# Optimization experiments

Hardware: AMD Instinct MI355X
Metric: run time of the kernel (lower is better)

## Reference

```python
import jax, jax.numpy as jnp
import numpy as np

B, TF, TP = 32, 2048, 256
FRAME_DIM, PHN_DIM, ATT_DIM = 768, 512, 512
LN_EPS = 1e-5


def setup_inputs() -> dict:
    key = jax.random.key(0)
    ks = jax.random.split(key, 9)
    frame_hidden = jax.random.normal(ks[0], (B, TF, FRAME_DIM), dtype=jnp.float32)
    phn_hidden = jax.random.normal(ks[1], (B, TP, PHN_DIM), dtype=jnp.float32)
    labels_att_mask = jax.random.randint(ks[2], (B, TP), 0, 2, dtype=jnp.int32)
    # ensure every row has at least one attended phoneme position
    labels_att_mask = labels_att_mask.at[:, 0].set(1)
    s_q = 1.0 / np.sqrt(FRAME_DIM)
    s_k = 1.0 / np.sqrt(PHN_DIM)
    Wq = jax.random.uniform(ks[3], (FRAME_DIM, ATT_DIM), jnp.float32, -s_q, s_q)
    bq = jax.random.uniform(ks[4], (ATT_DIM,), jnp.float32, -s_q, s_q)
    Wk = jax.random.uniform(ks[5], (PHN_DIM, ATT_DIM), jnp.float32, -s_k, s_k)
    bk = jax.random.uniform(ks[6], (ATT_DIM,), jnp.float32, -s_k, s_k)
    gamma = jnp.ones((2 * ATT_DIM,), jnp.float32)
    beta = jnp.zeros((2 * ATT_DIM,), jnp.float32)
    return {"frame_hidden": frame_hidden, "phn_hidden": phn_hidden,
            "labels_att_mask": labels_att_mask,
            "Wq": Wq, "bq": bq, "Wk": Wk, "bk": bk,
            "gamma": gamma, "beta": beta}


def _layer_norm(x, gamma, beta):
    mu = jnp.mean(x, axis=-1, keepdims=True)
    var = jnp.mean(jnp.square(x - mu), axis=-1, keepdims=True)
    return (x - mu) * jax.lax.rsqrt(var + LN_EPS) * gamma + beta


def reference(frame_hidden, phn_hidden, labels_att_mask, Wq, bq, Wk, bk, gamma, beta):
    q_frame = jnp.einsum('btf,fa->bta', frame_hidden, Wq) + bq   # [B,TF,A]
    k_phn = jnp.einsum('bpf,fa->bpa', phn_hidden, Wk) + bk       # [B,TP,A]
    energy = jnp.einsum('bta,bpa->btp', q_frame, k_phn)          # unscaled QK^T
    att_mask = (1.0 - labels_att_mask.astype(energy.dtype)) * -1000.0  # [B,TP]
    energy = energy + att_mask[:, None, :]
    att_matrix = jax.nn.softmax(energy, axis=-1)
    att_out = jnp.einsum('btp,bpa->bta', att_matrix, k_phn)      # [B,TF,A]
    att_out = jnp.concatenate([att_out, q_frame], axis=-1)       # [B,TF,2A]
    att_out = _layer_norm(att_out, gamma, beta)
    return (att_out, energy)
```

## Files before the change

### kernel.cpp

```cpp
#include <hip/hip_runtime.h>


typedef __bf16 bf16x8 __attribute__((ext_vector_type(8)));
typedef __bf16 bf16x4 __attribute__((ext_vector_type(4)));
typedef float  f32x4  __attribute__((ext_vector_type(4)));
typedef int    i32x4  __attribute__((ext_vector_type(4)));
typedef int    i32x2  __attribute__((ext_vector_type(2)));
typedef unsigned short u16;

__device__ __forceinline__ u16 f2b(float f) {
  union { float f; unsigned int i; } v; v.f = f;
  unsigned int u = v.i;
  return (u16)((u + 0x7FFFu + ((u >> 16) & 1u)) >> 16);
}
__device__ __forceinline__ bf16x8 ldfrag(const u16* p) {
  return __builtin_bit_cast(bf16x8, *(const i32x4*)p);
}
__device__ __forceinline__ f32x4 mfma16(bf16x8 a, bf16x8 b, f32x4 c) {
  return __builtin_amdgcn_mfma_f32_16x16x32_bf16(a, b, c, 0, 0, 0);
}
__device__ __forceinline__ void gl_lds16(const void* g, void* l) {
  __builtin_amdgcn_global_load_lds(
      (const __attribute__((address_space(1))) void*)g,
      (__attribute__((address_space(3))) void*)l, 16, 0, 0);
}

__global__ void transpose_f32_bf16(const float* __restrict__ in, u16* __restrict__ out,
                                   int R, int C) {
  __shared__ u16 tile[32][33];
  int c0 = blockIdx.x * 32, r0 = blockIdx.y * 32;
  int x = threadIdx.x, y = threadIdx.y;
#pragma unroll
  for (int i = 0; i < 32; i += 8) tile[y + i][x] = f2b(in[(size_t)(r0 + y + i) * C + c0 + x]);
  __syncthreads();
#pragma unroll
  for (int i = 0; i < 32; i += 8) out[(size_t)(c0 + y + i) * R + r0 + x] = tile[x][y + i];
}

__global__ void transpose_bf16(const u16* __restrict__ in, u16* __restrict__ out,
                               int R, int C, long inStride, long outStride) {
  __shared__ u16 tile[32][33];
  long bb = blockIdx.z;
  in  += bb * inStride;
  out += bb * outStride;
  int c0 = blockIdx.x * 32, r0 = blockIdx.y * 32;
  int x = threadIdx.x, y = threadIdx.y;
#pragma unroll
  for (int i = 0; i < 32; i += 8) tile[y + i][x] = in[(size_t)(r0 + y + i) * C + c0 + x];
  __syncthreads();
#pragma unroll
  for (int i = 0; i < 32; i += 8) out[(size_t)(c0 + y + i) * R + r0 + x] = tile[x][y + i];
}

__global__ __launch_bounds__(256, 2) void gemm_bias_bt(
    const float* __restrict__ A, const u16* __restrict__ Bt,
    const float* __restrict__ bias, u16* __restrict__ C, int M, int N, int K) {
  __shared__ __align__(16) u16 As[2][128][72];
  __shared__ __align__(16) u16 Bs[2][128][64];
  int tid = threadIdx.x, wave = tid >> 6, lane = tid & 63;
  int l = lane & 15, q = lane >> 4;
  int wr = wave >> 1, wc = wave & 1;

  int chunk = gridDim.x >> 3;
  int swz = (blockIdx.x & 7) * chunk + (blockIdx.x >> 3);
  int n0 = (swz & 3) * 128, m0 = (swz >> 2) * 128;

  int aRow = tid >> 4, aCol = (tid & 15) * 4;
  int NT = K >> 6;
  int sw = ((lane & 7) ^ (lane >> 3)) << 4;

  f32x4 acc[4][4];
#pragma unroll
  for (int mt = 0; mt < 4; mt++)
#pragma unroll
    for (int nt = 0; nt < 4; nt++) acc[mt][nt] = (f32x4)0.0f;
  f32x4 pf[8];

  auto stageB = [&](int buf, int kc) {
#pragma unroll
    for (int i = 0; i < 4; i++) {
      int rb = wave * 4 + i;
      int r  = rb * 8 + (lane >> 3);
      const char* src = (const char*)Bt + ((size_t)(n0 + r) * K + kc) * 2 + sw;
      gl_lds16(src, (char*)&Bs[buf][0][0] + rb * 1024);
    }
  };
  auto loadA = [&](int kc) {
#pragma unroll
    for (int i = 0; i < 8; i++)
      pf[i] = *(const f32x4*)&A[(size_t)(m0 + aRow + i * 16) * K + kc + aCol];
  };
  auto writeA = [&](int buf) {
#pragma unroll
    for (int i = 0; i < 8; i++) {
      bf16x4 h;
#pragma unroll
      for (int j = 0; j < 4; j++) h[j] = (__bf16)pf[i][j];
      *(i32x2*)&As[buf][aRow + i * 16][aCol] = __builtin_bit_cast(i32x2, h);
    }
  };

  stageB(0, 0);
  loadA(0);
  writeA(0);
  __syncthreads();

  for (int t = 0; t < NT; t++) {
    int cur = t & 1, nxt = cur ^ 1;
    bool more = (t + 1 < NT);
    if (more) { stageB(nxt, (t + 1) << 6); loadA((t + 1) << 6); }
#pragma unroll
    for (int ks = 0; ks < 64; ks += 32) {
      bf16x8 af[4], bv[4];
#pragma unroll
      for (int mt = 0; mt < 4; mt++) af[mt] = ldfrag(&As[cur][wr * 64 + mt * 16 + l][ks + q * 8]);
#pragma unroll
      for (int nt = 0; nt < 4; nt++) {
        int row = wc * 64 + nt * 16 + l;
        bv[nt] = ldfrag((const u16*)((const char*)&Bs[cur][0][0] + row * 128 +
                                     (((ks << 1) + q * 16) ^ ((l & 7) << 4))));
      }
#pragma unroll
      for (int mt = 0; mt < 4; mt++)
#pragma unroll
        for (int nt = 0; nt < 4; nt++) acc[mt][nt] = mfma16(af[mt], bv[nt], acc[mt][nt]);
    }
    if (more) writeA(nxt);
    __syncthreads();
  }

#pragma unroll
  for (int nt = 0; nt < 4; nt++) {
    int col = n0 + wc * 64 + nt * 16 + l;
    float bvv = bias[col];
#pragma unroll
    for (int mt = 0; mt < 4; mt++)
#pragma unroll
      for (int r = 0; r < 4; r++) {
        int row = m0 + wr * 64 + mt * 16 + q * 4 + r;
        C[(size_t)row * N + col] = f2b(acc[mt][nt][r] + bvv);
      }
  }
}

__global__ __launch_bounds__(256, 2) void attn_fused(
    const u16* __restrict__ Qbuf,
    const u16* __restrict__ Kp,
    const u16* __restrict__ KpT,
    const int* __restrict__ mask,
    const float* __restrict__ gamma, const float* __restrict__ beta,
    float* __restrict__ out0,
    float* __restrict__ out1) {
  __shared__ __align__(16) char smem[74752];
  u16* Ps   = (u16*)smem;
  u16* Kts0 = (u16*)(smem + 33792);

  int tid = threadIdx.x, wave = tid >> 6, lane = tid & 63;
  int l = lane & 15, q = lane >> 4;

  int chunk = gridDim.x >> 3;
  int swz = (blockIdx.x & 7) * chunk + (blockIdx.x >> 3);
  int m0 = (swz & 31) * 64, b = swz >> 5;

  const u16* Qb  = Qbuf + ((size_t)b * 2048 + m0) * 512;
  const u16* Kb  = Kp  + (size_t)b * 256 * 512;
  const u16* KTb = KpT + (size_t)b * 512 * 256;
  int sw = ((lane & 7) ^ (lane >> 3)) << 4;

  float madd[16];
#pragma unroll
  for (int nt = 0; nt < 16; nt++)
    madd[nt] = (float)(1 - mask[b * 256 + nt * 16 + l]) * -1000.0f;

  bf16x8 af[16];
#pragma unroll
  for (int t = 0; t < 8; t++)
#pragma unroll
    for (int s = 0; s < 2; s++)
      af[t * 2 + s] = ldfrag(&Qb[(size_t)(wave * 16 + l) * 512 + t * 64 + s * 32 + q * 8]);

  auto stageK = [&](int buf, int kc) {
#pragma unroll
    for (int i = 0; i < 8; i++) {
      int rb = wave * 8 + i;
      int r  = rb * 8 + (lane >> 3);
      const char* src = (const char*)Kb + ((size_t)r * 512 + kc) * 2 + sw;
      gl_lds16(src, smem + buf * 32768 + rb * 1024);
    }
  };

  f32x4 accE[16];
#pragma unroll
  for (int nt = 0; nt < 16; nt++) accE[nt] = (f32x4)0.0f;

  stageK(0, 0);
  __syncthreads();
#pragma unroll
  for (int t = 0; t < 8; t++) {
    int cur = t & 1;
    if (t < 7) stageK(cur ^ 1, (t + 1) * 64);
    const char* kb = smem + cur * 32768;
    __builtin_amdgcn_s_setprio(1);
#pragma unroll
    for (int s = 0; s < 2; s++) {
      bf16x8 a = af[t * 2 + s];
#pragma unroll
      for (int nt = 0; nt < 16; nt++) {
        int row = nt * 16 + l;
        bf16x8 bv = ldfrag((const u16*)(kb + row * 128 +
                                        ((s * 64 + q * 16) ^ ((l & 7) << 4))));
        accE[nt] = mfma16(a, bv, accE[nt]);
      }
    }
    __builtin_amdgcn_s_setprio(0);
    __syncthreads();
  }

  i32x4 kpf[4];
  auto loadKts = [&](int t) {
    int h = t >> 3, pc = (t & 7) * 32;
#pragma unroll
    for (int i = 0; i < 4; i++) {
      int r = (tid >> 2) + i * 64, c = (tid & 3) * 8;
      kpf[i] = *(const i32x4*)&KTb[(size_t)(h * 256 + r) * 256 + pc + c];
    }
  };
  auto writeKts = [&](int buf) {
#pragma unroll
    for (int i = 0; i < 4; i++) {
      int r = (tid >> 2) + i * 64, c = (tid & 3) * 8;
      *(i32x4*)&Kts0[(size_t)buf * 10240 + r * 40 + c] = kpf[i];
    }
  };
  loadKts(0);

  int rbase = m0 + wave * 16 + q * 4;
#pragma unroll
  for (int nt = 0; nt < 16; nt++)
#pragma unroll
    for (int r = 0; r < 4; r++) accE[nt][r] += madd[nt];

#pragma unroll
  for (int r = 0; r < 4; r++) {
    size_t rowoff = ((size_t)b * 2048 + rbase + r) * 256;
#pragma unroll
    for (int nt = 0; nt < 16; nt++) out1[rowoff + nt * 16 + l] = accE[nt][r];
  }

  float mx[4], sm[4], rs[4];
#pragma unroll
  for (int r = 0; r < 4; r++) mx[r] = -1e30f;
#pragma unroll
  for (int nt = 0; nt < 16; nt++)
#pragma unroll
    for (int r = 0; r < 4; r++) mx[r] = fmaxf(mx[r], accE[nt][r]);
#pragma unroll
  for (int off = 1; off < 16; off <<= 1)
#pragma unroll
    for (int r = 0; r < 4; r++) mx[r] = fmaxf(mx[r], __shfl_xor(mx[r], off));
#pragma unroll
  for (int r = 0; r < 4; r++) sm[r] = 0.0f;
#pragma unroll
  for (int nt = 0; nt < 16; nt++)
#pragma unroll
    for (int r = 0; r < 4; r++) {
      float p = __expf(accE[nt][r] - mx[r]);
      accE[nt][r] = p;
      sm[r] += p;
    }
#pragma unroll
  for (int off = 1; off < 16; off <<= 1)
#pragma unroll
    for (int r = 0; r < 4; r++) sm[r] += __shfl_xor(sm[r], off);
#pragma unroll
  for (int r = 0; r < 4; r++) rs[r] = 1.0f / sm[r];

#pragma unroll
  for (int r = 0; r < 4; r++)
#pragma unroll
    for (int nt = 0; nt < 16; nt++)
      Ps[(wave * 16 + q * 4 + r) * 264 + nt * 16 + l] = f2b(accE[nt][r] * rs[r]);

  writeKts(0);
  __syncthreads();

  f32x4 accO[32];
#pragma unroll
  for (int g = 0; g < 32; g++) accO[g] = (f32x4)0.0f;
#pragma unroll
  for (int t = 0; t < 16; t++) {
    int cur = t & 1, h = t >> 3, pc = (t & 7) * 32;
    if (t < 15) loadKts(t + 1);
    bf16x8 ps = ldfrag(&Ps[(wave * 16 + l) * 264 + pc + q * 8]);
    __builtin_amdgcn_s_setprio(1);
#pragma unroll
    for (int nt = 0; nt < 16; nt++) {
      bf16x8 bv = ldfrag(&Kts0[(size_t)cur * 10240 + (nt * 16 + l) * 40 + q * 8]);
      accO[h * 16 + nt] = mfma16(ps, bv, accO[h * 16 + nt]);
    }
    __builtin_amdgcn_s_setprio(0);
    if (t < 15) writeKts(cur ^ 1);
    __syncthreads();
  }

  float s1[4], s2[4];
#pragma unroll
  for (int r = 0; r < 4; r++) { s1[r] = 0.0f; s2[r] = 0.0f; }
#pragma unroll
  for (int g = 0; g < 32; g++)
#pragma unroll
    for (int r = 0; r < 4; r++) { float v = accO[g][r]; s1[r] += v; s2[r] += v * v; }
#pragma unroll
  for (int r = 0; r < 4; r++) {
    const u16* qr = Qb + (size_t)(wave * 16 + q * 4 + r) * 512;
#pragma unroll
    for (int p = 0; p < 4; p++) {
      bf16x8 qv = ldfrag(&qr[p * 128 + l * 8]);
#pragma unroll
      for (int j = 0; j < 8; j++) { float v = (float)qv[j]; s1[r] += v; s2[r] += v * v; }
    }
  }
#pragma unroll
  for (int off = 1; off < 16; off <<= 1)
#pragma unroll
    for (int r = 0; r < 4; r++) {
      s1[r] += __shfl_xor(s1[r], off);
      s2[r] += __shfl_xor(s2[r], off);
    }
#pragma unroll
  for (int r = 0; r < 4; r++) {
    float mean = s1[r] * (1.0f / 1024.0f);
    float var  = s2[r] * (1.0f / 1024.0f) - mean * mean;
    float rstd = rsqrtf(var + 1e-5f);
    size_t rowbase = ((size_t)b * 2048 + rbase + r) * 1024;
#pragma unroll
    for (int g = 0; g < 32; g++) {
      int col = g * 16 + l;
      out0[rowbase + col] = (accO[g][r] - mean) * rstd * gamma[col] + beta[col];
    }
    const u16* qr = Qb + (size_t)(wave * 16 + q * 4 + r) * 512;
#pragma unroll
    for (int p = 0; p < 4; p++) {
      bf16x8 qv = ldfrag(&qr[p * 128 + l * 8]);
      float ov[8];
#pragma unroll
      for (int j = 0; j < 8; j++) {
        int col = 512 + p * 128 + l * 8 + j;
        ov[j] = ((float)qv[j] - mean) * rstd * gamma[col] + beta[col];
      }
      *(f32x4*)&out0[rowbase + 512 + p * 128 + l * 8] = *(f32x4*)&ov[0];
      *(f32x4*)&out0[rowbase + 516 + p * 128 + l * 8] = *(f32x4*)&ov[4];
    }
  }
}

extern "C" void kernel_launch(void* const* d_in, const int* in_sizes, int n_in,
                              void* d_out, int out_size, void* d_ws, size_t ws_size,
                              hipStream_t stream) {
  (void)in_sizes; (void)n_in; (void)out_size; (void)ws_size;
  const float* frame = (const float*)d_in[0];
  const float* phn   = (const float*)d_in[1];
  const int*   msk   = (const int*)d_in[2];
  const float* Wq    = (const float*)d_in[3];
  const float* bq    = (const float*)d_in[4];
  const float* Wk    = (const float*)d_in[5];
  const float* bk    = (const float*)d_in[6];
  const float* gamma = (const float*)d_in[7];
  const float* beta  = (const float*)d_in[8];

  u16* ws   = (u16*)d_ws;
  u16* WqT  = ws;
  u16* WkT  = ws + 393216;
  u16* Qbuf = ws + 655360;
  u16* Kp   = ws + 34209792;
  u16* KpT  = ws + 38404096;

  float* out0 = (float*)d_out;
  float* out1 = out0 + (size_t)32 * 2048 * 1024;

  transpose_f32_bf16<<<dim3(16, 24, 1), dim3(32, 8, 1), 0, stream>>>(Wq, WqT, 768, 512);
  transpose_f32_bf16<<<dim3(16, 16, 1), dim3(32, 8, 1), 0, stream>>>(Wk, WkT, 512, 512);
  gemm_bias_bt<<<dim3(2048, 1, 1), dim3(256, 1, 1), 0, stream>>>(frame, WqT, bq, Qbuf, 65536, 512, 768);
  gemm_bias_bt<<<dim3(256, 1, 1), dim3(256, 1, 1), 0, stream>>>(phn, WkT, bk, Kp, 8192, 512, 512);
  transpose_bf16<<<dim3(16, 8, 32), dim3(32, 8, 1), 0, stream>>>(Kp, KpT, 256, 512, 131072, 131072);
  attn_fused<<<dim3(1024, 1, 1), dim3(256, 1, 1), 0, stream>>>(Qbuf, Kp, KpT, msk, gamma, beta, out0, out1);
}
```

Measured before the change: 670.8 us.

## Fuse Q projection GEMM into attention kernel, keeping Q tile in LDS

Drops the standalone Q-projection GEMM and its bf16 Q buffer in global memory. Each 512-thread block now computes its 64x512 Q tile from fp32 frame inputs directly into swizzled LDS, then reuses that tile for QK^T and for the layer norm. The work is split across 8 waves by rows and column groups, so row max, sum and layer-norm statistics need cross-wave reductions through LDS. This removes the write and re-read of the Q intermediate and one kernel launch. In exchange it uses 160 KB of LDS per block, which limits residency to one block per CU, and it adds extra barriers.

```diff
diff --git a/kernel.cpp b/kernel.cpp
--- a/kernel.cpp
+++ b/kernel.cpp
@@ -13,7 +13,7 @@
   unsigned int u = v.i;
   return (u16)((u + 0x7FFFu + ((u >> 16) & 1u)) >> 16);
 }
-__device__ __forceinline__ bf16x8 ldfrag(const u16* p) {
+__device__ __forceinline__ bf16x8 ldfrag(const void* p) {
   return __builtin_bit_cast(bf16x8, *(const i32x4*)p);
 }
 __device__ __forceinline__ f32x4 mfma16(bf16x8 a, bf16x8 b, f32x4 c) {
@@ -60,11 +60,9 @@
   int tid = threadIdx.x, wave = tid >> 6, lane = tid & 63;
   int l = lane & 15, q = lane >> 4;
   int wr = wave >> 1, wc = wave & 1;
-
   int chunk = gridDim.x >> 3;
   int swz = (blockIdx.x & 7) * chunk + (blockIdx.x >> 3);
   int n0 = (swz & 3) * 128, m0 = (swz >> 2) * 128;
-
   int aRow = tid >> 4, aCol = (tid & 15) * 4;
   int NT = K >> 6;
   int sw = ((lane & 7) ^ (lane >> 3)) << 4;
@@ -117,8 +115,8 @@
 #pragma unroll
       for (int nt = 0; nt < 4; nt++) {
         int row = wc * 64 + nt * 16 + l;
-        bv[nt] = ldfrag((const u16*)((const char*)&Bs[cur][0][0] + row * 128 +
-                                     (((ks << 1) + q * 16) ^ ((l & 7) << 4))));
+        bv[nt] = ldfrag((const char*)&Bs[cur][0][0] + row * 128 +
+                        (((ks << 1) + q * 16) ^ ((l & 7) << 4)));
       }
 #pragma unroll
       for (int mt = 0; mt < 4; mt++)
@@ -143,55 +141,130 @@
   }
 }
 
-__global__ __launch_bounds__(256, 2) void attn_fused(
-    const u16* __restrict__ Qbuf,
+#define QS_OFF 0
+#define R1_OFF 65536
+#define PS_OFF 65536
+#define KT_OFF 98304
+#define AS_OFF 131072
+#define SX_OFF 131072
+#define SS_OFF 132096
+#define S1A_OFF 65536
+#define S2A_OFF 66560
+
+__global__ __launch_bounds__(512, 2) void fused_qattn(
+    const float* __restrict__ frame,
+    const u16* __restrict__ WqT,
+    const float* __restrict__ bq,
     const u16* __restrict__ Kp,
     const u16* __restrict__ KpT,
     const int* __restrict__ mask,
     const float* __restrict__ gamma, const float* __restrict__ beta,
     float* __restrict__ out0,
     float* __restrict__ out1) {
-  __shared__ __align__(16) char smem[74752];
-  u16* Ps   = (u16*)smem;
-  u16* Kts0 = (u16*)(smem + 33792);
+  __shared__ __align__(16) char smem[163840];
 
   int tid = threadIdx.x, wave = tid >> 6, lane = tid & 63;
   int l = lane & 15, q = lane >> 4;
+  int rg = (wave & 1) * 32;
 
   int chunk = gridDim.x >> 3;
   int swz = (blockIdx.x & 7) * chunk + (blockIdx.x >> 3);
   int m0 = (swz & 31) * 64, b = swz >> 5;
 
-  const u16* Qb  = Qbuf + ((size_t)b * 2048 + m0) * 512;
+  const float* Fb = frame + ((size_t)b * 2048 + m0) * 768;
   const u16* Kb  = Kp  + (size_t)b * 256 * 512;
   const u16* KTb = KpT + (size_t)b * 512 * 256;
-  int sw = ((lane & 7) ^ (lane >> 3)) << 4;
-
-  float madd[16];
-#pragma unroll
-  for (int nt = 0; nt < 16; nt++)
-    madd[nt] = (float)(1 - mask[b * 256 + nt * 16 + l]) * -1000.0f;
-
-  bf16x8 af[16];
-#pragma unroll
-  for (int t = 0; t < 8; t++)
-#pragma unroll
-    for (int s = 0; s < 2; s++)
-      af[t * 2 + s] = ldfrag(&Qb[(size_t)(wave * 16 + l) * 512 + t * 64 + s * 32 + q * 8]);
-
+
+  auto qs_ptr = [&](int row, int colb) -> u16* {
+    return (u16*)(smem + QS_OFF + row * 1024 + (colb ^ ((row & 7) << 4)));
+  };
+
+  {
+    int cgA = (wave >> 1) * 128;
+    f32x4 accq[2][8];
+#pragma unroll
+    for (int mt = 0; mt < 2; mt++)
+#pragma unroll
+      for (int nt = 0; nt < 8; nt++) accq[mt][nt] = (f32x4)0.0f;
+    f32x4 pf;
+
+    int bsw = ((lane & 3) ^ ((lane >> 2) & 3)) << 4;
+    auto stageB = [&](int buf, int kc) {
+#pragma unroll
+      for (int i = 0; i < 4; i++) {
+        int c = wave * 4 + i;
+        int row = c * 16 + (lane >> 2);
+        const char* src = (const char*)WqT + ((size_t)row * 768 + kc) * 2 + bsw;
+        gl_lds16(src, smem + R1_OFF + buf * 32768 + c * 1024);
+      }
+    };
+    auto loadA = [&](int kc) {
+      pf = *(const f32x4*)&Fb[(size_t)(tid >> 3) * 768 + kc + (tid & 7) * 4];
+    };
+    auto writeA = [&](int buf) {
+      bf16x4 h;
+#pragma unroll
+      for (int j = 0; j < 4; j++) h[j] = (__bf16)pf[j];
+      *(i32x2*)(smem + AS_OFF + buf * 5120 + (tid >> 3) * 80 + (tid & 7) * 8) =
+          __builtin_bit_cast(i32x2, h);
+    };
+
+    stageB(0, 0); loadA(0); writeA(0);
+    __syncthreads();
+    for (int t = 0; t < 24; t++) {
+      int cur = t & 1;
+      bool more = (t < 23);
+      if (more) { stageB(cur ^ 1, (t + 1) * 32); loadA((t + 1) * 32); }
+      bf16x8 af[2], bv[8];
+#pragma unroll
+      for (int mt = 0; mt < 2; mt++)
+        af[mt] = ldfrag(smem + AS_OFF + cur * 5120 + (rg + mt * 16 + l) * 80 + q * 16);
+#pragma unroll
+      for (int nt = 0; nt < 8; nt++) {
+        int row = cgA + nt * 16 + l;
+        bv[nt] = ldfrag(smem + R1_OFF + cur * 32768 + row * 64 +
+                        ((q * 16) ^ ((l & 3) << 4)));
+      }
+      __builtin_amdgcn_s_setprio(1);
+#pragma unroll
+      for (int mt = 0; mt < 2; mt++)
+#pragma unroll
+        for (int nt = 0; nt < 8; nt++) accq[mt][nt] = mfma16(af[mt], bv[nt], accq[mt][nt]);
+      __builtin_amdgcn_s_setprio(0);
+      if (more) writeA(cur ^ 1);
+      __syncthreads();
+    }
+#pragma unroll
+    for (int nt = 0; nt < 8; nt++) {
+      int col = cgA + nt * 16 + l;
+      float bqv = bq[col];
+#pragma unroll
+      for (int mt = 0; mt < 2; mt++)
+#pragma unroll
+        for (int r = 0; r < 4; r++) {
+          int row = rg + mt * 16 + q * 4 + r;
+          *qs_ptr(row, col * 2) = f2b(accq[mt][nt][r] + bqv);
+        }
+    }
+  }
+
+  int cg1 = (wave >> 1) * 64;
+  f32x4 accE[2][4];
+#pragma unroll
+  for (int mt = 0; mt < 2; mt++)
+#pragma unroll
+    for (int nt = 0; nt < 4; nt++) accE[mt][nt] = (f32x4)0.0f;
+
+  int ksw = ((lane & 7) ^ (lane >> 3)) << 4;
   auto stageK = [&](int buf, int kc) {
 #pragma unroll
-    for (int i = 0; i < 8; i++) {
-      int rb = wave * 8 + i;
-      int r  = rb * 8 + (lane >> 3);
-      const char* src = (const char*)Kb + ((size_t)r * 512 + kc) * 2 + sw;
-      gl_lds16(src, smem + buf * 32768 + rb * 1024);
+    for (int i = 0; i < 4; i++) {
+      int c = wave * 4 + i;
+      int row = c * 8 + (lane >> 3);
+      const char* src = (const char*)Kb + ((size_t)row * 512 + kc) * 2 + ksw;
+      gl_lds16(src, smem + R1_OFF + buf * 32768 + c * 1024);
     }
   };
-
-  f32x4 accE[16];
-#pragma unroll
-  for (int nt = 0; nt < 16; nt++) accE[nt] = (f32x4)0.0f;
 
   stageK(0, 0);
   __syncthreads();
@@ -199,159 +272,260 @@
   for (int t = 0; t < 8; t++) {
     int cur = t & 1;
     if (t < 7) stageK(cur ^ 1, (t + 1) * 64);
-    const char* kb = smem + cur * 32768;
     __builtin_amdgcn_s_setprio(1);
 #pragma unroll
     for (int s = 0; s < 2; s++) {
-      bf16x8 a = af[t * 2 + s];
-#pragma unroll
-      for (int nt = 0; nt < 16; nt++) {
-        int row = nt * 16 + l;
-        bf16x8 bv = ldfrag((const u16*)(kb + row * 128 +
-                                        ((s * 64 + q * 16) ^ ((l & 7) << 4))));
-        accE[nt] = mfma16(a, bv, accE[nt]);
-      }
+      bf16x8 af[2], bv[4];
+#pragma unroll
+      for (int mt = 0; mt < 2; mt++)
+        af[mt] = ldfrag(qs_ptr(rg + mt * 16 + l, t * 128 + s * 64 + q * 16));
+#pragma unroll
+      for (int nt = 0; nt < 4; nt++) {
+        int row = cg1 + nt * 16 + l;
+        bv[nt] = ldfrag(smem + R1_OFF + cur * 32768 + row * 128 +
+                        ((s * 64 + q * 16) ^ ((l & 7) << 4)));
+      }
+#pragma unroll
+      for (int mt = 0; mt < 2; mt++)
+#pragma unroll
+        for (int nt = 0; nt < 4; nt++) accE[mt][nt] = mfma16(af[mt], bv[nt], accE[mt][nt]);
     }
     __builtin_amdgcn_s_setprio(0);
     __syncthreads();
   }
 
-  i32x4 kpf[4];
-  auto loadKts = [&](int t) {
-    int h = t >> 3, pc = (t & 7) * 32;
+  float madd[4];
+#pragma unroll
+  for (int nt = 0; nt < 4; nt++)
+    madd[nt] = (float)(1 - mask[b * 256 + cg1 + nt * 16 + l]) * -1000.0f;
+#pragma unroll
+  for (int mt = 0; mt < 2; mt++)
+#pragma unroll
+    for (int nt = 0; nt < 4; nt++)
+#pragma unroll
+      for (int r = 0; r < 4; r++) accE[mt][nt][r] += madd[nt];
+
+  int rbase = m0 + rg + q * 4;
+#pragma unroll
+  for (int mt = 0; mt < 2; mt++)
+#pragma unroll
+    for (int r = 0; r < 4; r++) {
+      size_t ro = ((size_t)b * 2048 + rbase + mt * 16 + r) * 256;
+#pragma unroll
+      for (int nt = 0; nt < 4; nt++) out1[ro + cg1 + nt * 16 + l] = accE[mt][nt][r];
+    }
+
+  float* SX = (float*)(smem + SX_OFF);
+  float* SS = (float*)(smem + SS_OFF);
+  float mx[2][4], sm[2][4], rs[2][4];
+#pragma unroll
+  for (int mt = 0; mt < 2; mt++)
+#pragma unroll
+    for (int r = 0; r < 4; r++) {
+      float m = -1e30f;
+#pragma unroll
+      for (int nt = 0; nt < 4; nt++) m = fmaxf(m, accE[mt][nt][r]);
+      mx[mt][r] = m;
+    }
+#pragma unroll
+  for (int off = 1; off < 16; off <<= 1)
+#pragma unroll
+    for (int mt = 0; mt < 2; mt++)
+#pragma unroll
+      for (int r = 0; r < 4; r++) mx[mt][r] = fmaxf(mx[mt][r], __shfl_xor(mx[mt][r], off));
+  if (l == 0)
+#pragma unroll
+    for (int mt = 0; mt < 2; mt++)
+#pragma unroll
+      for (int r = 0; r < 4; r++) SX[wave * 32 + mt * 16 + q * 4 + r] = mx[mt][r];
+  __syncthreads();
+#pragma unroll
+  for (int mt = 0; mt < 2; mt++)
+#pragma unroll
+    for (int r = 0; r < 4; r++) {
+      float m = mx[mt][r];
+#pragma unroll
+      for (int pw = 0; pw < 8; pw += 2) {
+        int w2 = (wave & 1) + pw;
+        if (w2 != wave) m = fmaxf(m, SX[w2 * 32 + mt * 16 + q * 4 + r]);
+      }
+      mx[mt][r] = m;
+      sm[mt][r] = 0.0f;
+    }
+#pragma unroll
+  for (int mt = 0; mt < 2; mt++)
+#pragma unroll
+    for (int nt = 0; nt < 4; nt++)
+#pragma unroll
+      for (int r = 0; r < 4; r++) {
+        float p = __expf(accE[mt][nt][r] - mx[mt][r]);
+        accE[mt][nt][r] = p;
+        sm[mt][r] += p;
+      }
+#pragma unroll
+  for (int off = 1; off < 16; off <<= 1)
+#pragma unroll
+    for (int mt = 0; mt < 2; mt++)
+#pragma unroll
+      for (int r = 0; r < 4; r++) sm[mt][r] += __shfl_xor(sm[mt][r], off);
+  if (l == 0)
+#pragma unroll
+    for (int mt = 0; mt < 2; mt++)
+#pragma unroll
+      for (int r = 0; r < 4; r++) SS[wave * 32 + mt * 16 + q * 4 + r] = sm[mt][r];
+  __syncthreads();
+#pragma unroll
+  for (int mt = 0; mt < 2; mt++)
+#pragma unroll
+    for (int r = 0; r < 4; r++) {
+      float s = sm[mt][r];
+#pragma unroll
+      for (int pw = 0; pw < 8; pw += 2) {
+        int w2 = (wave & 1) + pw;
+        if (w2 != wave) s += SS[w2 * 32 + mt * 16 + q * 4 + r];
+      }
+      rs[mt][r] = 1.0f / s;
+    }
+#pragma unroll
+  for (int mt = 0; mt < 2; mt++)
+#pragma unroll
+    for (int r = 0; r < 4; r++) {
+      int row = rg + mt * 16 + q * 4 + r;
+#pragma unroll
+      for (int nt = 0; nt < 4; nt++) {
+        int col = cg1 + nt * 16 + l;
+        *(u16*)(smem + PS_OFF + row * 512 + ((col * 2) ^ ((row & 7) << 4))) =
+            f2b(accE[mt][nt][r] * rs[mt][r]);
+      }
+    }
+
+  int og3 = (wave >> 1) * 128;
+  int tsw = ((lane & 3) ^ ((lane >> 2) & 3)) << 4;
+  auto stageKt = [&](int buf, int pc) {
 #pragma unroll
     for (int i = 0; i < 4; i++) {
-      int r = (tid >> 2) + i * 64, c = (tid & 3) * 8;
-      kpf[i] = *(const i32x4*)&KTb[(size_t)(h * 256 + r) * 256 + pc + c];
+      int c = wave * 4 + i;
+      int row = c * 16 + (lane >> 2);
+      const char* src = (const char*)KTb + ((size_t)row * 256 + pc) * 2 + tsw;
+      gl_lds16(src, smem + KT_OFF + buf * 32768 + c * 1024);
     }
   };
-  auto writeKts = [&](int buf) {
-#pragma unroll
-    for (int i = 0; i < 4; i++) {
-      int r = (tid >> 2) + i * 64, c = (tid & 3) * 8;
-      *(i32x4*)&Kts0[(size_t)buf * 10240 + r * 40 + c] = kpf[i];
-    }
-  };
-  loadKts(0);
-
-  int rbase = m0 + wave * 16 + q * 4;
-#pragma unroll
-  for (int nt = 0; nt < 16; nt++)
-#pragma unroll
-    for (int r = 0; r < 4; r++) accE[nt][r] += madd[nt];
-
-#pragma unroll
-  for (int r = 0; r < 4; r++) {
-    size_t rowoff = ((size_t)b * 2048 + rbase + r) * 256;
-#pragma unroll
-    for (int nt = 0; nt < 16; nt++) out1[rowoff + nt * 16 + l] = accE[nt][r];
-  }
-
-  float mx[4], sm[4], rs[4];
-#pragma unroll
-  for (int r = 0; r < 4; r++) mx[r] = -1e30f;
-#pragma unroll
-  for (int nt = 0; nt < 16; nt++)
-#pragma unroll
-    for (int r = 0; r < 4; r++) mx[r] = fmaxf(mx[r], accE[nt][r]);
-#pragma unroll
-  for (int off = 1; off < 16; off <<= 1)
-#pragma unroll
-    for (int r = 0; r < 4; r++) mx[r] = fmaxf(mx[r], __shfl_xor(mx[r], off));
-#pragma unroll
-  for (int r = 0; r < 4; r++) sm[r] = 0.0f;
-#pragma unroll
-  for (int nt = 0; nt < 16; nt++)
-#pragma unroll
-    for (int r = 0; r < 4; r++) {
-      float p = __expf(accE[nt][r] - mx[r]);
-      accE[nt][r] = p;
-      sm[r] += p;
-    }
-#pragma unroll
-  for (int off = 1; off < 16; off <<= 1)
-#pragma unroll
-    for (int r = 0; r < 4; r++) sm[r] += __shfl_xor(sm[r], off);
-#pragma unroll
-  for (int r = 0; r < 4; r++) rs[r] = 1.0f / sm[r];
-
-#pragma unroll
-  for (int r = 0; r < 4; r++)
-#pragma unroll
-    for (int nt = 0; nt < 16; nt++)
-      Ps[(wave * 16 + q * 4 + r) * 264 + nt * 16 + l] = f2b(accE[nt][r] * rs[r]);
-
-  writeKts(0);
-  __syncthreads();
-
-  f32x4 accO[32];
-#pragma unroll
-  for (int g = 0; g < 32; g++) accO[g] = (f32x4)0.0f;
-#pragma unroll
-  for (int t = 0; t < 16; t++) {
-    int cur = t & 1, h = t >> 3, pc = (t & 7) * 32;
-    if (t < 15) loadKts(t + 1);
-    bf16x8 ps = ldfrag(&Ps[(wave * 16 + l) * 264 + pc + q * 8]);
+  stageKt(0, 0);
+  __syncthreads();
+
+  f32x4 accO[2][8];
+#pragma unroll
+  for (int mt = 0; mt < 2; mt++)
+#pragma unroll
+    for (int nt = 0; nt < 8; nt++) accO[mt][nt] = (f32x4)0.0f;
+#pragma unroll
+  for (int t = 0; t < 8; t++) {
+    int cur = t & 1, pc = t * 32;
+    if (t < 7) stageKt(cur ^ 1, (t + 1) * 32);
+    bf16x8 ps[2], bv[8];
+#pragma unroll
+    for (int mt = 0; mt < 2; mt++) {
+      int row = rg + mt * 16 + l;
+      ps[mt] = ldfrag(smem + PS_OFF + row * 512 + ((pc * 2 + q * 16) ^ ((l & 7) << 4)));
+    }
     __builtin_amdgcn_s_setprio(1);
 #pragma unroll
-    for (int nt = 0; nt < 16; nt++) {
-      bf16x8 bv = ldfrag(&Kts0[(size_t)cur * 10240 + (nt * 16 + l) * 40 + q * 8]);
-      accO[h * 16 + nt] = mfma16(ps, bv, accO[h * 16 + nt]);
-    }
+    for (int nt = 0; nt < 8; nt++) {
+      int row = og3 + nt * 16 + l;
+      bv[nt] = ldfrag(smem + KT_OFF + cur * 32768 + row * 64 +
+                      ((q * 16) ^ ((l & 3) << 4)));
+    }
+#pragma unroll
+    for (int mt = 0; mt < 2; mt++)
+#pragma unroll
+      for (int nt = 0; nt < 8; nt++) accO[mt][nt] = mfma16(ps[mt], bv[nt], accO[mt][nt]);
     __builtin_amdgcn_s_setprio(0);
-    if (t < 15) writeKts(cur ^ 1);
     __syncthreads();
   }
 
-  float s1[4], s2[4];
-#pragma unroll
-  for (int r = 0; r < 4; r++) { s1[r] = 0.0f; s2[r] = 0.0f; }
-#pragma unroll
-  for (int g = 0; g < 32; g++)
-#pragma unroll
-    for (int r = 0; r < 4; r++) { float v = accO[g][r]; s1[r] += v; s2[r] += v * v; }
-#pragma unroll
-  for (int r = 0; r < 4; r++) {
-    const u16* qr = Qb + (size_t)(wave * 16 + q * 4 + r) * 512;
-#pragma unroll
-    for (int p = 0; p < 4; p++) {
-      bf16x8 qv = ldfrag(&qr[p * 128 + l * 8]);
-#pragma unroll
-      for (int j = 0; j < 8; j++) { float v = (float)qv[j]; s1[r] += v; s2[r] += v * v; }
-    }
-  }
+  float s1[2][4], s2[2][4];
+#pragma unroll
+  for (int mt = 0; mt < 2; mt++)
+#pragma unroll
+    for (int r = 0; r < 4; r++) { s1[mt][r] = 0.0f; s2[mt][r] = 0.0f; }
+#pragma unroll
+  for (int mt = 0; mt < 2; mt++)
+#pragma unroll
+    for (int nt = 0; nt < 8; nt++)
+#pragma unroll
+      for (int r = 0; r < 4; r++) {
+        float v = accO[mt][nt][r];
+        s1[mt][r] += v; s2[mt][r] += v * v;
+      }
+#pragma unroll
+  for (int mt = 0; mt < 2; mt++)
+#pragma unroll
+    for (int r = 0; r < 4; r++) {
+      int row = rg + mt * 16 + q * 4 + r;
+      bf16x8 qv = ldfrag(qs_ptr(row, (og3 + l * 8) * 2));
+#pragma unroll
+      for (int j = 0; j < 8; j++) {
+        float v = (float)qv[j];
+        s1[mt][r] += v; s2[mt][r] += v * v;
+      }
+    }
 #pragma unroll
   for (int off = 1; off < 16; off <<= 1)
 #pragma unroll
-    for (int r = 0; r < 4; r++) {
-      s1[r] += __shfl_xor(s1[r], off);
-      s2[r] += __shfl_xor(s2[r], off);
-    }
-#pragma unroll
-  for (int r = 0; r < 4; r++) {
-    float mean = s1[r] * (1.0f / 1024.0f);
-    float var  = s2[r] * (1.0f / 1024.0f) - mean * mean;
-    float rstd = rsqrtf(var + 1e-5f);
-    size_t rowbase = ((size_t)b * 2048 + rbase + r) * 1024;
-#pragma unroll
-    for (int g = 0; g < 32; g++) {
-      int col = g * 16 + l;
-      out0[rowbase + col] = (accO[g][r] - mean) * rstd * gamma[col] + beta[col];
-    }
-    const u16* qr = Qb + (size_t)(wave * 16 + q * 4 + r) * 512;
-#pragma unroll
-    for (int p = 0; p < 4; p++) {
-      bf16x8 qv = ldfrag(&qr[p * 128 + l * 8]);
+    for (int mt = 0; mt < 2; mt++)
+#pragma unroll
+      for (int r = 0; r < 4; r++) {
+        s1[mt][r] += __shfl_xor(s1[mt][r], off);
+        s2[mt][r] += __shfl_xor(s2[mt][r], off);
+      }
+  float* S1A = (float*)(smem + S1A_OFF);
+  float* S2A = (float*)(smem + S2A_OFF);
+  if (l == 0)
+#pragma unroll
+    for (int mt = 0; mt < 2; mt++)
+#pragma unroll
+      for (int r = 0; r < 4; r++) {
+        S1A[wave * 32 + mt * 16 + q * 4 + r] = s1[mt][r];
+        S2A[wave * 32 + mt * 16 + q * 4 + r] = s2[mt][r];
+      }
+  __syncthreads();
+#pragma unroll
+  for (int mt = 0; mt < 2; mt++)
+#pragma unroll
+    for (int r = 0; r < 4; r++) {
+#pragma unroll
+      for (int pw = 0; pw < 8; pw += 2) {
+        int w2 = (wave & 1) + pw;
+        if (w2 != wave) {
+          s1[mt][r] += S1A[w2 * 32 + mt * 16 + q * 4 + r];
+          s2[mt][r] += S2A[w2 * 32 + mt * 16 + q * 4 + r];
+        }
+      }
+    }
+#pragma unroll
+  for (int mt = 0; mt < 2; mt++)
+#pragma unroll
+    for (int r = 0; r < 4; r++) {
+      float mean = s1[mt][r] * (1.0f / 1024.0f);
+      float var  = s2[mt][r] * (1.0f / 1024.0f) - mean * mean;
+      float rstd = rsqrtf(var + 1e-5f);
+      int row = rg + mt * 16 + q * 4 + r;
+      size_t rowbase = ((size_t)b * 2048 + m0 + row) * 1024;
+#pragma unroll
+      for (int nt = 0; nt < 8; nt++) {
+        int col = og3 + nt * 16 + l;
+        out0[rowbase + col] = (accO[mt][nt][r] - mean) * rstd * gamma[col] + beta[col];
+      }
+      bf16x8 qv = ldfrag(qs_ptr(row, (og3 + l * 8) * 2));
       float ov[8];
 #pragma unroll
       for (int j = 0; j < 8; j++) {
-        int col = 512 + p * 128 + l * 8 + j;
+        int col = 512 + og3 + l * 8 + j;
         ov[j] = ((float)qv[j] - mean) * rstd * gamma[col] + beta[col];
       }
-      *(f32x4*)&out0[rowbase + 512 + p * 128 + l * 8] = *(f32x4*)&ov[0];
-      *(f32x4*)&out0[rowbase + 516 + p * 128 + l * 8] = *(f32x4*)&ov[4];
-    }
-  }
+      *(f32x4*)&out0[rowbase + 512 + og3 + l * 8]     = *(f32x4*)&ov[0];
+      *(f32x4*)&out0[rowbase + 512 + og3 + l * 8 + 4] = *(f32x4*)&ov[4];
+    }
 }
 
 extern "C" void kernel_launch(void* const* d_in, const int* in_sizes, int n_in,
@@ -371,17 +545,16 @@
   u16* ws   = (u16*)d_ws;
   u16* WqT  = ws;
   u16* WkT  = ws + 393216;
-  u16* Qbuf = ws + 655360;
-  u16* Kp   = ws + 34209792;
-  u16* KpT  = ws + 38404096;
+  u16* Kp   = ws + 655360;
+  u16* KpT  = ws + 4849664;
 
   float* out0 = (float*)d_out;
   float* out1 = out0 + (size_t)32 * 2048 * 1024;
 
   transpose_f32_bf16<<<dim3(16, 24, 1), dim3(32, 8, 1), 0, stream>>>(Wq, WqT, 768, 512);
   transpose_f32_bf16<<<dim3(16, 16, 1), dim3(32, 8, 1), 0, stream>>>(Wk, WkT, 512, 512);
-  gemm_bias_bt<<<dim3(2048, 1, 1), dim3(256, 1, 1), 0, stream>>>(frame, WqT, bq, Qbuf, 65536, 512, 768);
   gemm_bias_bt<<<dim3(256, 1, 1), dim3(256, 1, 1), 0, stream>>>(phn, WkT, bk, Kp, 8192, 512, 512);
   transpose_bf16<<<dim3(16, 8, 32), dim3(32, 8, 1), 0, stream>>>(Kp, KpT, 256, 512, 131072, 131072);
-  attn_fused<<<dim3(1024, 1, 1), dim3(256, 1, 1), 0, stream>>>(Qbuf, Kp, KpT, msk, gamma, beta, out0, out1);
-}
+  fused_qattn<<<dim3(1024, 1, 1), dim3(512, 1, 1), 0, stream>>>(
+      frame, WqT, bq, Kp, KpT, msk, gamma, beta, out0, out1);
+}
```

Result: no change. 676.5 us (+0.9%).
